# Kernel optimization log

Hardware: AMD Instinct MI355X
Metric: run time of the kernel (lower is better)

Reference implementation:

```python
import jax, jax.numpy as jnp
import numpy as np

DIM = 2048; H = 16; DK = 128; DV = 128; SEQ = 2048; KCONV = 4
KEY_DIM = H * DK; VAL_DIM = H * DV
EPS_L2 = 1e-6; EPS_RMS = 1e-6; SP_THRESH = 20.0


def setup_inputs() -> dict:
    key = jax.random.key(0)
    ks = jax.random.split(key, 20)
    f = jnp.float32
    def w(k, shape, scale):
        return jax.random.normal(k, shape, f) * scale
    s_in = DIM ** -0.5
    return {
        "x": jax.random.normal(ks[0], (1, SEQ, DIM), f),
        "ve": jax.random.normal(ks[1], (1, SEQ, H, DV), f),
        "sa_lambdas": jnp.array([0.7, 0.3], f),
        "Wq": w(ks[2], (DIM, KEY_DIM), s_in),
        "Wk": w(ks[3], (DIM, KEY_DIM), s_in),
        "Wv": w(ks[4], (DIM, VAL_DIM), s_in),
        "conv_q": w(ks[5], (KEY_DIM, KCONV), 0.5),
        "conv_k": w(ks[6], (KEY_DIM, KCONV), 0.5),
        "conv_v": w(ks[7], (VAL_DIM, KCONV), 0.5),
        "Wf1": w(ks[8], (DIM, DV), s_in),
        "Wf2": w(ks[9], (DV, KEY_DIM), DV ** -0.5),
        "Wb": w(ks[10], (DIM, H), s_in),
        "A_log": jnp.log(jax.random.uniform(ks[11], (H,), f, 1.0, 16.0)),
        "dt_bias": jnp.zeros((KEY_DIM,), f),
        "Wg1": w(ks[12], (DIM, DV), s_in),
        "Wg2": w(ks[13], (DV, VAL_DIM), DV ** -0.5),
        "bg2": jnp.zeros((VAL_DIM,), f),
        "norm_w": jnp.ones((DV,), f),
        "Wo": w(ks[14], (VAL_DIM, DIM), VAL_DIM ** -0.5),
    }


def _short_conv_silu(u, w):
    # u: [b, s, c], w: [c, K]; causal depthwise conv + silu
    s = u.shape[1]
    up = jnp.pad(u, ((0, 0), (w.shape[1] - 1, 0), (0, 0)))
    y = sum(up[:, i:i + s, :] * w[:, i] for i in range(w.shape[1]))
    return jax.nn.silu(y)


def _l2norm(t):
    return t * jax.lax.rsqrt(jnp.sum(t * t, axis=-1, keepdims=True) + EPS_L2)


def _forward(x, ve, sa_lambdas, Wq, Wk, Wv, conv_q, conv_k, conv_v,
             Wf1, Wf2, Wb, A_log, dt_bias, Wg1, Wg2, bg2, norm_w, Wo):
    b, s, _ = x.shape  # b == 1
    q = _short_conv_silu(x @ Wq, conv_q).reshape(b, s, H, DK)
    k = _short_conv_silu(x @ Wk, conv_k).reshape(b, s, H, DK)
    v = _short_conv_silu(x @ Wv, conv_v).reshape(b, s, H, DV)
    v = sa_lambdas[0] * v + sa_lambdas[1] * ve
    # KDA gate: per-(head, key-dim) log decay
    g = ((x @ Wf1) @ Wf2).reshape(b, s, H, DK) + dt_bias.reshape(H, DK)
    sp = jnp.where(g > SP_THRESH, g, jnp.log1p(jnp.exp(jnp.minimum(g, SP_THRESH))))
    glog = -jnp.exp(A_log)[None, None, :, None] * sp  # [b,s,h,dk]
    beta = jax.nn.sigmoid(x @ Wb)  # [b,s,h]
    # l2-normalize q,k; scale q by dk^-0.5 (chunk_kda default scale)
    qn = _l2norm(q) * (DK ** -0.5)
    kn = _l2norm(k)
    # gated delta-rule recurrence over time (b==1, squeeze batch)
    def step(S, inp):
        qt, kt, vt, gt, bt = inp  # [h,dk],[h,dk],[h,dv],[h,dk],[h]
        S = S * jnp.exp(gt)[..., None]  # per-key-channel decay
        pred = jnp.einsum('hk,hkv->hv', kt, S)
        vt_new = bt[:, None] * (vt - pred)
        S = S + kt[:, :, None] * vt_new[:, None, :]
        ot = jnp.einsum('hk,hkv->hv', qt, S)
        return S, ot
    S0 = jnp.zeros((H, DK, DV), x.dtype)
    _, o = jax.lax.scan(step, S0, (qn[0], kn[0], v[0], glog[0], beta[0]))
    o = o[None]  # [1,s,h,dv]
    # sigmoid-gated RMSNorm over head_v_dim
    gate = ((x @ Wg1) @ Wg2 + bg2).reshape(b, s, H, DV)
    var = jnp.mean(o * o, axis=-1, keepdims=True)
    o = o * jax.lax.rsqrt(var + EPS_RMS) * norm_w
    o = o * jax.nn.sigmoid(gate)
    return o.reshape(b, s, VAL_DIM) @ Wo  # [1,s,dim]


def reference(x, ve, sa_lambdas, Wq, Wk, Wv, conv_q, conv_k, conv_v,
              Wf1, Wf2, Wb, A_log, dt_bias, Wg1, Wg2, bg2, norm_w, Wo):
    return _forward(x, ve, sa_lambdas, Wq, Wk, Wv, conv_q, conv_k, conv_v,
                    Wf1, Wf2, Wb, A_log, dt_bias, Wg1, Wg2, bg2, norm_w, Wo)
```

## Files before the change

kernel.cpp:

```cpp
#include <hip/hip_runtime.h>
#include <hip/hip_bf16.h>
#include <stdint.h>
#include <stddef.h>

#define SEQL 2048
#define DIMSZ 2048
#define HN 16
#define DKD 128
#define DVD 128
#define QSCALE 0.08838834764831843f

typedef __attribute__((ext_vector_type(4))) float f32x4;
typedef __attribute__((ext_vector_type(2))) float f32x2;
typedef __attribute__((ext_vector_type(8))) short bf16x8;

__device__ __forceinline__ float sigmoid_f(float x) { return 1.f / (1.f + __expf(-x)); }
__device__ __forceinline__ float bf2f(short s) {
  union { float f; unsigned int u; } t; t.u = ((unsigned int)(unsigned short)s) << 16; return t.f;
}

#define BM 128
#define BN 128
#define BKK 64

// ... 113 lines not shown
          const int kc = ks * 4 + l4;
          a[m2][ks] = *(const bf16x8*)(lds + cb + la * 64 + (kc ^ (la & 7)) * 8);
        }
    }
#pragma unroll
    for (int ks = 0; ks < 2; ++ks) {
      const int lb = NQ * 64 + wn * 16 + l15;
      const int kc = ks * 4 + l4;
      b[ks] = *(const bf16x8*)(lds + cb + 16384 + lb * 64 + (kc ^ (lb & 7)) * 8);
    }
    __builtin_amdgcn_s_setprio(1);
#pragma unroll
    for (int m2 = 0; m2 < 4; ++m2)
#pragma unroll
      for (int ks = 0; ks < 2; ++ks)
        acc[MQ * 4 + m2][NQ] = __builtin_amdgcn_mfma_f32_16x16x32_bf16(
            a[m2][ks], b[ks], acc[MQ * 4 + m2][NQ], 0, 0, 0);
    __builtin_amdgcn_s_setprio(0);
  };

  stage_a(0, 0); stage_a(1, 0); stage_b(0, 0); stage_b(1, 0); stage_b(2, 0);

  for (int t = 0; t < NT; ++t) {
    const size_t cb = (size_t)(t & 1) * 28672;
    stage_a(0, t + 1);
    asm volatile("s_waitcnt vmcnt(4)" ::: "memory");
    __builtin_amdgcn_s_barrier();
    __builtin_amdgcn_sched_barrier(0);
    phase(cb, 0, 0, true);
    __builtin_amdgcn_s_barrier();
    stage_a(1, t + 1);
    asm volatile("s_waitcnt vmcnt(5)" ::: "memory");
    __builtin_amdgcn_s_barrier();
    __builtin_amdgcn_sched_barrier(0);
    phase(cb, 0, 1, false);
    __builtin_amdgcn_s_barrier();
    stage_b(0, t + 1);
    asm volatile("s_waitcnt vmcnt(5)" ::: "memory");
    __builtin_amdgcn_s_barrier();
    __builtin_amdgcn_sched_barrier(0);
    phase(cb, 0, 2, false);
    __builtin_amdgcn_s_barrier();
    stage_b(1, t + 1);
    __builtin_amdgcn_s_barrier();
    __builtin_amdgcn_sched_barrier(0);
    phase(cb, 1, 0, true);
    __builtin_amdgcn_s_barrier();
    stage_b(2, t + 1);
    __builtin_amdgcn_s_barrier();
    __builtin_amdgcn_sched_barrier(0);
    phase(cb, 1, 1, false);
    __builtin_amdgcn_s_barrier();
    __builtin_amdgcn_s_barrier();
    __builtin_amdgcn_sched_barrier(0);
    phase(cb, 1, 2, false);
    __builtin_amdgcn_s_barrier();
  }
  asm volatile("s_waitcnt vmcnt(0)" ::: "memory");

#pragma unroll
  for (int mi = 0; mi < 8; ++mi)
#pragma unroll
    for (int nq = 0; nq < 3; ++nq) {
      const int row = m0 + wm * 128 + mi * 16 + l4 * 4;
      const int col = n0 + nq * 64 + wn * 16 + l15;
#pragma unroll
      for (int r = 0; r < 4; ++r)
        Cb[(size_t)(row + r) * N + col] = __float2bfloat16(acc[mi][nq][r]);
    }
}

__global__ __launch_bounds__(256) void gemm_btsplit(
    const __hip_bfloat16* __restrict__ Ah, const __hip_bfloat16* __restrict__ Al,
    const __hip_bfloat16* __restrict__ Bh, const __hip_bfloat16* __restrict__ Bl,
    float* __restrict__ C, int M, int N, int lda, int ldb, int klen)
{
  __shared__ __hip_bfloat16 Ash[BM * BKK];
  __shared__ __hip_bfloat16 Asl[BM * BKK];
  __shared__ __hip_bfloat16 Bsh[BN * BKK];
  __shared__ __hip_bfloat16 Bsl[BN * BKK];
  const int tid = threadIdx.x;
  const int lane = tid & 63;
  const int w = tid >> 6;
  const int wm = w >> 1, wn = w & 1;
  const int m0 = blockIdx.y * BM, n0 = blockIdx.x * BN;
  const int l15 = lane & 15, l4 = lane >> 4;
  const int kbase = blockIdx.z * klen;

  f32x4 acc[4][4] = {};

  for (int k0 = kbase; k0 < kbase + klen; k0 += BKK) {
#pragma unroll
    for (int i = 0; i < 4; ++i) {
      const int c = (w * 4 + i) * 64 + lane;
      const int row = c >> 3;
      const int colb = (c & 7) * 8;
      const size_t go = (size_t)(m0 + row) * lda + k0 + colb;
      const size_t gn = (size_t)(n0 + row) * ldb + k0 + colb;
      __builtin_amdgcn_global_load_lds(
          (const __attribute__((address_space(1))) void*)(Ah + go),
          (__attribute__((address_space(3))) void*)(Ash + (size_t)c * 8), 16, 0, 0);
      __builtin_amdgcn_global_load_lds(
          (const __attribute__((address_space(1))) void*)(Al + go),
          (__attribute__((address_space(3))) void*)(Asl + (size_t)c * 8), 16, 0, 0);
      __builtin_amdgcn_global_load_lds(
          (const __attribute__((address_space(1))) void*)(Bh + gn),
          (__attribute__((address_space(3))) void*)(Bsh + (size_t)c * 8), 16, 0, 0);
      __builtin_amdgcn_global_load_lds(
          (const __attribute__((address_space(1))) void*)(Bl + gn),
          (__attribute__((address_space(3))) void*)(Bsl + (size_t)c * 8), 16, 0, 0);
    }
    __syncthreads();
#pragma unroll
    for (int kk = 0; kk < BKK; kk += 32) {
      bf16x8 afh[4], afl[4], bfh[4], bfl[4];
#pragma unroll
      for (int mi = 0; mi < 4; ++mi) {
        const int ao = (wm * 64 + mi * 16 + l15) * BKK + kk + l4 * 8;
        afh[mi] = *(const bf16x8*)(Ash + ao);
        afl[mi] = *(const bf16x8*)(Asl + ao);
      }
#pragma unroll
      for (int ni = 0; ni < 4; ++ni) {
        const int bo = (wn * 64 + ni * 16 + l15) * BKK + kk + l4 * 8;
        bfh[ni] = *(const bf16x8*)(Bsh + bo);
        bfl[ni] = *(const bf16x8*)(Bsl + bo);
      }
#pragma unroll
      for (int mi = 0; mi < 4; ++mi)
#pragma unroll
        for (int ni = 0; ni < 4; ++ni) {
          acc[mi][ni] = __builtin_amdgcn_mfma_f32_16x16x32_bf16(afh[mi], bfh[ni], acc[mi][ni], 0, 0, 0);
          acc[mi][ni] = __builtin_amdgcn_mfma_f32_16x16x32_bf16(afh[mi], bfl[ni], acc[mi][ni], 0, 0, 0);
          acc[mi][ni] = __builtin_amdgcn_mfma_f32_16x16x32_bf16(afl[mi], bfh[ni], acc[mi][ni], 0, 0, 0);
        }
    }
    __syncthreads();
  }

  float* Cz = C + (size_t)blockIdx.z * M * N;
#pragma unroll
  for (int mi = 0; mi < 4; ++mi) {
#pragma unroll
    for (int ni = 0; ni < 4; ++ni) {
      const int row = m0 + wm * 64 + mi * 16 + l4 * 4;
      const int col = n0 + wn * 64 + ni * 16 + l15;
#pragma unroll
      for (int r = 0; r < 4; ++r)
        Cz[(size_t)(row + r) * N + col] = acc[mi][ni][r];
    }
  }
}

__global__ __launch_bounds__(256) void transpose4_kernel(
    const float* __restrict__ Wq, const float* __restrict__ Wk,
    const float* __restrict__ Wv, const float* __restrict__ Wo,
    __hip_bfloat16* __restrict__ WqkvT, __hip_bfloat16* __restrict__ WoT)
{
  __shared__ float tile[32][33];
  const int z = blockIdx.z;
  const float* in = (z == 0) ? Wq : (z == 1) ? Wk : (z == 2) ? Wv : Wo;
  __hip_bfloat16* outT = (z < 3) ? (WqkvT + (size_t)z * 2048 * 2048) : WoT;
  const int c0 = blockIdx.x * 32, r0 = blockIdx.y * 32;
  const int tc = threadIdx.x & 31, tr = threadIdx.x >> 5;
#pragma unroll
  for (int i = 0; i < 4; ++i)
    tile[tr + i * 8][tc] = in[(size_t)(r0 + tr + i * 8) * 2048 + c0 + tc];
  __syncthreads();
#pragma unroll
  for (int i = 0; i < 4; ++i)
    outT[(size_t)(c0 + tr + i * 8) * 2048 + r0 + tc] = __float2bfloat16(tile[tc][tr + i * 8]);
}

__global__ __launch_bounds__(256) void transpose_fg1_kernel(
    const float* __restrict__ Wf1, const float* __restrict__ Wg1,
    __hip_bfloat16* __restrict__ hT, __hip_bfloat16* __restrict__ lT)
{
  __shared__ float tile[32][33];
  const int z = blockIdx.z;
  const float* in = z ? Wg1 : Wf1;
  const size_t base = (size_t)z * 128 * 2048;
  const int c0 = blockIdx.x * 32, r0 = blockIdx.y * 32;
  const int tc = threadIdx.x & 31, tr = threadIdx.x >> 5;
#pragma unroll
  for (int i = 0; i < 4; ++i)
    tile[tr + i * 8][tc] = in[(size_t)(r0 + tr + i * 8) * 128 + c0 + tc];
  __syncthreads();
#pragma unroll
  for (int i = 0; i < 4; ++i) {
    float val = tile[tc][tr + i * 8];
    __hip_bfloat16 h = __float2bfloat16(val);
    size_t oi = base + (size_t)(c0 + tr + i * 8) * 2048 + r0 + tc;
    hT[oi] = h;
    lT[oi] = z ? __float2bfloat16(0.f) : __float2bfloat16(val - __bfloat162float(h));
  }
}

__global__ __launch_bounds__(256) void transpose_f2g2_kernel(
    const float* __restrict__ Wf2, const float* __restrict__ Wg2,
    __hip_bfloat16* __restrict__ f2h, __hip_bfloat16* __restrict__ f2l,
    __hip_bfloat16* __restrict__ g2h)
{
  __shared__ float tile[32][33];
  const int z = blockIdx.z;
  const float* in = z ? Wg2 : Wf2;
  const int c0 = blockIdx.x * 32, r0 = blockIdx.y * 32;
  const int tc = threadIdx.x & 31, tr = threadIdx.x >> 5;
#pragma unroll
  for (int i = 0; i < 4; ++i)
    tile[tr + i * 8][tc] = in[(size_t)(r0 + tr + i * 8) * 2048 + c0 + tc];
  __syncthreads();
#pragma unroll
  for (int i = 0; i < 4; ++i) {
    float val = tile[tc][tr + i * 8];
    __hip_bfloat16 h = __float2bfloat16(val);
    size_t oi = (size_t)(c0 + tr + i * 8) * 128 + r0 + tc;
    if (z == 0) { f2h[oi] = h; f2l[oi] = __float2bfloat16(val - __bfloat162float(h)); }
    else g2h[oi] = h;
  }
}

__global__ __launch_bounds__(256) void cast_split_kernel(
    const float* __restrict__ in, __hip_bfloat16* __restrict__ hi,
    __hip_bfloat16* __restrict__ lo, int n4)
{
  int idx = blockIdx.x * 256 + threadIdx.x;
  if (idx >= n4) return;
  f32x4 v = *(const f32x4*)(in + (size_t)idx * 4);
  union { __hip_bfloat16 b[4]; unsigned long long u; } ph, pl;
#pragma unroll
  for (int j = 0; j < 4; ++j) {
    float f = v[j];
    __hip_bfloat16 hh = __float2bfloat16(f);
    ph.b[j] = hh;
    pl.b[j] = __float2bfloat16(f - __bfloat162float(hh));
  }
  *(unsigned long long*)((char*)hi + (size_t)idx * 8) = ph.u;
  if (lo) *(unsigned long long*)((char*)lo + (size_t)idx * 8) = pl.u;
}

__global__ __launch_bounds__(256) void reduce8_kernel(
    const float* __restrict__ part, __hip_bfloat16* __restrict__ hi,
    __hip_bfloat16* __restrict__ lo, int n4, size_t chunk)
{
  int idx = blockIdx.x * 256 + threadIdx.x;
  if (idx >= n4) return;
  f32x4 a = *(const f32x4*)(part + (size_t)idx * 4);
#pragma unroll
  for (int z = 1; z < 8; ++z) {
    f32x4 b = *(const f32x4*)(part + z * chunk + (size_t)idx * 4);
    a.x += b.x; a.y += b.y; a.z += b.z; a.w += b.w;
  }
  union { __hip_bfloat16 b[4]; unsigned long long u; } ph, pl;
#pragma unroll
  for (int j = 0; j < 4; ++j) {
    float f = a[j];
    __hip_bfloat16 hh = __float2bfloat16(f);
    ph.b[j] = hh;
    pl.b[j] = __float2bfloat16(f - __bfloat162float(hh));
  }
  *(unsigned long long*)((char*)hi + (size_t)idx * 8) = ph.u;
  if (lo) *(unsigned long long*)((char*)lo + (size_t)idx * 8) = pl.u;
}

__global__ __launch_bounds__(256) void beta_kernel(
    const float* __restrict__ x, const float* __restrict__ Wb, float* __restrict__ betaT)
{
  int idx = blockIdx.x * 256 + threadIdx.x;
  int s = idx >> 4, h = idx & 15;
  const float* xr = x + (size_t)s * DIMSZ;
  float acc = 0.f;
  for (int d = 0; d < DIMSZ; d += 4) {
    f32x4 xv = *(const f32x4*)(xr + d);
    acc = fmaf(xv.x, Wb[(size_t)(d + 0) * HN + h], acc);
    acc = fmaf(xv.y, Wb[(size_t)(d + 1) * HN + h], acc);
    acc = fmaf(xv.z, Wb[(size_t)(d + 2) * HN + h], acc);
    acc = fmaf(xv.w, Wb[(size_t)(d + 3) * HN + h], acc);
  }
  betaT[(size_t)h * SEQL + s] = 1.f / (1.f + expf(-acc));
}

#define SL20(r, d) ((r) * 160 + ((d) >> 4) * 20 + ((d) & 15))

__global__ __launch_bounds__(256) void kda_pref(
    const __hip_bfloat16* __restrict__ qkv, const float* __restrict__ ve,
    const float* __restrict__ lam,
    const float* __restrict__ cwq, const float* __restrict__ cwk, const float* __restrict__ cwv,
    const float* __restrict__ gbuf,
    const float* __restrict__ dtb, const float* __restrict__ A_log,
    const float* __restrict__ betaT,
    __hip_bfloat16* __restrict__ Xgh, __hip_bfloat16* __restrict__ KTh,
    float* __restrict__ uvS, float* __restrict__ olocS, float* __restrict__ Pg)
{
  __shared__ float GL2[32 * 160];
  __shared__ float kL2[32 * 160];
  __shared__ float qL2[32 * 132];
  __shared__ float vL2[32 * 128];
  __shared__ float ALB[32][33];
  __shared__ float Bdiag[32], betaL[32];
  __shared__ float csumW[4 * 128];

  const int bid = blockIdx.x;
  const int h = bid >> 6, cc = bid & 63;
  const int tid = threadIdx.x;
  const int w = tid >> 6, lane = tid & 63;
  const size_t hc = (size_t)h * 64 + cc;
  const float Aexp = __expf(A_log[h]);

  {
    const int c = lane * 2;
    const int r0g = cc * 32 + w * 8;
    const int cg = h * 128 + c;

    f32x4 wq0 = *(const f32x4*)(cwq + (size_t)cg * 4), wq1 = *(const f32x4*)(cwq + (size_t)(cg + 1) * 4);
    f32x4 wk0 = *(const f32x4*)(cwk + (size_t)cg * 4), wk1 = *(const f32x4*)(cwk + (size_t)(cg + 1) * 4);
    f32x4 wv0 = *(const f32x4*)(cwv + (size_t)cg * 4), wv1 = *(const f32x4*)(cwv + (size_t)(cg + 1) * 4);
    f32x2 dt2 = *(const f32x2*)(dtb + cg);
    const float l0 = lam[0], l1 = lam[1];

    f32x2 xqr[11], xkr[11], xvr[11];
#pragma unroll
    for (int i = 0; i < 11; ++i) {
      const int sr = r0g - 3 + i;
      if (sr >= 0) {
        const size_t ro = (size_t)sr * 6144 + cg;
        unsigned int uq = *(const unsigned int*)(qkv + ro);
        unsigned int uk = *(const unsigned int*)(qkv + 2048 + ro);
        unsigned int uv2 = *(const unsigned int*)(qkv + 4096 + ro);
        xqr[i].x = bf2f((short)uq);   xqr[i].y = bf2f((short)(uq >> 16));
        xkr[i].x = bf2f((short)uk);   xkr[i].y = bf2f((short)(uk >> 16));
        xvr[i].x = bf2f((short)uv2);  xvr[i].y = bf2f((short)(uv2 >> 16));
      } else {
        xqr[i].x = xqr[i].y = xkr[i].x = xkr[i].y = xvr[i].x = xvr[i].y = 0.f;
      }
    }

    float gl0[8], gl1[8];
#pragma unroll
    for (int i = 0; i < 8; ++i) {
      const int rr = r0g + i;
      const int lr = w * 8 + i;
      float aq0 = 0, aq1 = 0, ak0 = 0, ak1 = 0, av0 = 0, av1 = 0;
#pragma unroll
      for (int j = 0; j < 4; ++j) {
        aq0 = fmaf(xqr[i + j].x, wq0[j], aq0); aq1 = fmaf(xqr[i + j].y, wq1[j], aq1);
        ak0 = fmaf(xkr[i + j].x, wk0[j], ak0); ak1 = fmaf(xkr[i + j].y, wk1[j], ak1);
        av0 = fmaf(xvr[i + j].x, wv0[j], av0); av1 = fmaf(xvr[i + j].y, wv1[j], av1);
      }
      float yq0 = aq0 * sigmoid_f(aq0), yq1 = aq1 * sigmoid_f(aq1);
      float yk0 = ak0 * sigmoid_f(ak0), yk1 = ak1 * sigmoid_f(ak1);
      float yv0 = av0 * sigmoid_f(av0), yv1 = av1 * sigmoid_f(av1);

      f32x2 vev = *(const f32x2*)(ve + ((size_t)rr * HN + h) * 128 + c);
      float v0 = l0 * yv0 + l1 * vev.x;
      float v1 = l0 * yv1 + l1 * vev.y;

      float ssq = yq0 * yq0 + yq1 * yq1;
      float ssk = yk0 * yk0 + yk1 * yk1;
#pragma unroll
      for (int off = 32; off > 0; off >>= 1) {
        ssq += __shfl_xor(ssq, off);
        ssk += __shfl_xor(ssk, off);
      }
      float rq = rsqrtf(ssq + 1e-6f) * QSCALE;
      float rk = rsqrtf(ssk + 1e-6f);

      f32x2 kk; kk.x = yk0 * rk; kk.y = yk1 * rk;
      f32x2 qq; qq.x = yq0 * rq; qq.y = yq1 * rq;
      f32x2 vv; vv.x = v0; vv.y = v1;
      *(f32x2*)&kL2[SL20(lr, c)] = kk;
      *(f32x2*)&qL2[lr * 132 + c] = qq;
      *(f32x2*)&vL2[lr * 128 + c] = vv;

      f32x2 gv = *(const f32x2*)(gbuf + (size_t)rr * 2048 + cg);
      float g0 = gv.x + dt2.x, g1 = gv.y + dt2.y;
      float sp0 = (g0 > 20.f) ? g0 : log1pf(__expf(fminf(g0, 20.f)));
      float sp1 = (g1 > 20.f) ? g1 : log1pf(__expf(fminf(g1, 20.f)));
      gl0[i] = -Aexp * sp0;
      gl1[i] = -Aexp * sp1;
    }
    {
      float r0 = 0.f, r1 = 0.f;
#pragma unroll
      for (int i = 0; i < 8; ++i) { r0 += gl0[i]; gl0[i] = r0; r1 += gl1[i]; gl1[i] = r1; }
      csumW[w * 128 + c] = r0;
      csumW[w * 128 + c + 1] = r1;
    }
    if (tid < 32) betaL[tid] = betaT[(size_t)h * SEQL + cc * 32 + tid];
    __syncthreads();
    {
      float p0 = 0.f, p1 = 0.f;
      for (int wp = 0; wp < w; ++wp) { p0 += csumW[wp * 128 + c]; p1 += csumW[wp * 128 + c + 1]; }
#pragma unroll
      for (int i = 0; i < 8; ++i) {
        f32x2 gg; gg.x = gl0[i] + p0; gg.y = gl1[i] + p1;
        *(f32x2*)&GL2[SL20(w * 8 + i, c)] = gg;
      }
    }
  }
  __syncthreads();

  {
    const int tg = lane >> 3, s8 = lane & 7;
    const int tt = w * 8 + tg;
    const int ds = s8 * 20;

    float Gt[16], kt[16], qt[16];
#pragma unroll
    for (int j = 0; j < 16; j += 4) {
      *(f32x4*)&Gt[j] = *(const f32x4*)&GL2[tt * 160 + ds + j];
      *(f32x4*)&kt[j] = *(const f32x4*)&kL2[tt * 160 + ds + j];
      *(f32x4*)&qt[j] = *(const f32x4*)&qL2[tt * 132 + s8 * 16 + j];
    }
    {
      float sA = 0.f, sB = 0.f;
#pragma unroll
      for (int j = 0; j < 16; ++j) { sA = fmaf(kt[j], kt[j], sA); sB = fmaf(qt[j], kt[j], sB); }
      sA += __shfl_xor(sA, 1); sA += __shfl_xor(sA, 2); sA += __shfl_xor(sA, 4);
      sB += __shfl_xor(sB, 1); sB += __shfl_xor(sB, 2); sB += __shfl_xor(sB, 4);
      if (s8 == 0) { ALB[tt][tt] = sA; Bdiag[tt] = sB; }
    }
    const int ibound = w * 8 + 7;
    for (int i = 0; i < ibound; ++i) {
      if (i < tt) {
        float sA = 0.f, sB = 0.f;
#pragma unroll
        for (int jj = 0; jj < 4; ++jj) {
          f32x4 Gi = *(const f32x4*)&GL2[i * 160 + ds + jj * 4];
          f32x4 ki = *(const f32x4*)&kL2[i * 160 + ds + jj * 4];
#pragma unroll
          for (int u = 0; u < 4; ++u) {
            float e = __expf(Gt[jj * 4 + u] - Gi[u]);
            float kid = ki[u] * e;
            sA = fmaf(kt[jj * 4 + u], kid, sA);
            sB = fmaf(qt[jj * 4 + u], kid, sB);
          }
        }
        sA += __shfl_xor(sA, 1); sA += __shfl_xor(sA, 2); sA += __shfl_xor(sA, 4);
        sB += __shfl_xor(sB, 1); sB += __shfl_xor(sB, 2); sB += __shfl_xor(sB, 4);
        if (s8 == 0) { ALB[tt][i] = sA; ALB[i][tt] = sB; }
      }
    }
  }
  __syncthreads();

  const int col = tid & 127, half = tid >> 7;
  const size_t rowbase = (size_t)(cc * 32) * 2048 + h * 128 + col;
  const int rbase = half * 16;
  {
    const float g31 = GL2[SL20(31, col)];
    size_t kb = hc * 4096 + (size_t)col * 32;
#pragma unroll
    for (int i = 0; i < 16; ++i) {
      int r = rbase + i;
      float kv = kL2[SL20(r, col)] * __expf(g31 - GL2[SL20(r, col)]);
      KTh[kb + r] = __float2bfloat16(kv);
    }
  }

  if (half == 0) {
    float expg[32];
#pragma unroll
    for (int r = 0; r < 32; ++r) expg[r] = __expf(GL2[SL20(r, col)]);

    float uvr[32], wr[32];
#pragma unroll
    for (int r = 0; r < 32; ++r) {
      float suv = 0.f, sw = 0.f;
#pragma unroll
      for (int j = 0; j < 32; ++j) {
        if (j < r) { float a = ALB[r][j]; suv = fmaf(a, uvr[j], suv); sw = fmaf(a, wr[j], sw); }
      }
      float br = betaL[r];
      float khr = kL2[SL20(r, col)] * expg[r];
      uvr[r] = br * (vL2[r * 128 + col] - suv);
      wr[r] = br * (khr - sw);
      uvS[rowbase + (size_t)r * 2048] = uvr[r];
      Xgh[hc * 8192 + (size_t)(32 + r) * 128 + col] = __float2bfloat16(wr[r]);
    }

#pragma unroll
    for (int r = 0; r < 32; ++r) {
      float qtv = qL2[r * 132 + col] * expg[r];
      float ol = 0.f;
#pragma unroll
      for (int j = 0; j < 32; ++j) {
        if (j < r) { float b = ALB[j][r]; qtv = fmaf(-b, wr[j], qtv); ol = fmaf(b, uvr[j], ol); }
      }
      { float b = Bdiag[r]; qtv = fmaf(-b, wr[r], qtv); ol = fmaf(b, uvr[r], ol); }
      Xgh[hc * 8192 + (size_t)r * 128 + col] = __float2bfloat16(qtv);
      olocS[rowbase + (size_t)r * 2048] = ol;
    }
    Pg[hc * 128 + col] = expg[31];
  }
}

#define STP 136
#define UTP 40

struct ChunkOps {
  bf16x8 ah[4];
  bf16x8 kah[2];
  f32x4 pvv[2];
  float pB[4];
};

__global__ __launch_bounds__(256) void kda_seq(
    const __hip_bfloat16* __restrict__ Xgh, const __hip_bfloat16* __restrict__ KTh,
    const float* __restrict__ uvS, const float* __restrict__ olocS,
    const float* __restrict__ Pg, float* __restrict__ obuf)
{
  __shared__ __hip_bfloat16 STh[16 * STP], STl[16 * STP];
  __shared__ __hip_bfloat16 UTh[16 * UTP];
  const int tid = threadIdx.x;
  const int w = tid >> 6, lane = tid & 63, l15 = lane & 15, l4 = lane >> 4;
  const int h = blockIdx.x >> 3, vq = blockIdx.x & 7;
  const int v0 = vq * 16;
  const int r0 = (w & 1) * 16 + l4 * 4;
  const int isO = (w < 2);

  for (int i = tid; i < 16 * STP; i += 256) {
    STh[i] = __float2bfloat16(0.f);
    STl[i] = __float2bfloat16(0.f);
  }
  __syncthreads();

  f32x4 S[2] = {};

  auto loadops = [&](ChunkOps& o, int c) {
    const size_t hc = (size_t)h * 64 + c;
    const __hip_bfloat16* xh = Xgh + hc * 8192 + (size_t)(w * 16 + l15) * 128 + l4 * 8;
#pragma unroll
    for (int kk = 0; kk < 4; ++kk) o.ah[kk] = *(const bf16x8*)(xh + kk * 32);
    const float* pb = (isO ? olocS : uvS) + (size_t)(c * 32 + r0) * 2048 + h * 128 + v0 + l15;
#pragma unroll
    for (int r = 0; r < 4; ++r) o.pB[r] = pb[(size_t)r * 2048];
#pragma unroll
    for (int mi = 0; mi < 2; ++mi) {
      const int kd = (w * 2 + mi) * 16;
      o.kah[mi] = *(const bf16x8*)(KTh + hc * 4096 + (size_t)(kd + l15) * 32 + l4 * 8);
      o.pvv[mi] = *(const f32x4*)(Pg + hc * 128 + kd + l4 * 4);
    }
  };

  auto body = [&](ChunkOps& o, int c) {
    f32x4 Y = {};
#pragma unroll
    for (int kk = 0; kk < 4; ++kk) {
      const int so = l15 * STP + kk * 32 + l4 * 8;
      bf16x8 bh = *(const bf16x8*)(STh + so);
      bf16x8 bl = *(const bf16x8*)(STl + so);
      Y = __builtin_amdgcn_mfma_f32_16x16x32_bf16(o.ah[kk], bh, Y, 0, 0, 0);
      Y = __builtin_amdgcn_mfma_f32_16x16x32_bf16(o.ah[kk], bl, Y, 0, 0, 0);
    }

    if (isO) {
      size_t ob = (size_t)(c * 32 + r0) * 2048 + h * 128 + v0 + l15;
#pragma unroll
      for (int r = 0; r < 4; ++r)
        obuf[ob + (size_t)r * 2048] = Y[r] + o.pB[r];
    } else {
      union { __hip_bfloat16 b[4]; unsigned long long u; } uh;
#pragma unroll
      for (int r = 0; r < 4; ++r)
        uh.b[r] = __float2bfloat16(o.pB[r] - Y[r]);
      *(unsigned long long*)(UTh + l15 * UTP + r0) = uh.u;
    }
    __syncthreads();

#pragma unroll
    for (int mi = 0; mi < 2; ++mi) S[mi] *= o.pvv[mi];
    {
      bf16x8 ubh = *(const bf16x8*)(UTh + l15 * UTP + l4 * 8);
#pragma unroll
      for (int mi = 0; mi < 2; ++mi)
        S[mi] = __builtin_amdgcn_mfma_f32_16x16x32_bf16(o.kah[mi], ubh, S[mi], 0, 0, 0);
    }

#pragma unroll
    for (int mi = 0; mi < 2; ++mi) {
      const int kd0 = (w * 2 + mi) * 16 + l4 * 4;
      union { __hip_bfloat16 b[4]; unsigned long long u; } sh, sl;
#pragma unroll
      for (int r = 0; r < 4; ++r) {
        __hip_bfloat16 hh = __float2bfloat16(S[mi][r]);
        sh.b[r] = hh;
        sl.b[r] = __float2bfloat16(S[mi][r] - __bfloat162float(hh));
      }
      *(unsigned long long*)(STh + l15 * STP + kd0) = sh.u;
      *(unsigned long long*)(STl + l15 * STP + kd0) = sl.u;
    }
    __syncthreads();
  };

  ChunkOps A_, B_;
  loadops(A_, 0);
  for (int c = 0; c < 64; c += 2) {
    loadops(B_, c + 1);
    body(A_, c);
    if (c + 2 < 64) loadops(A_, c + 2);
    body(B_, c + 1);
  }
}

__global__ __launch_bounds__(256) void rmsgate_kernel(
    const float* __restrict__ o, const float* __restrict__ gate,
    const float* __restrict__ bg2, const float* __restrict__ norm_w,
    __hip_bfloat16* __restrict__ og)
{
  int row = blockIdx.x * 4 + (threadIdx.x >> 6);
  int lane = threadIdx.x & 63;
  int s = row >> 4, h = row & 15;
  int j = lane * 2;
  const float* p = o + (size_t)row * 128 + j;
  f32x2 v = *(const f32x2*)p;
  float ss = v.x * v.x + v.y * v.y;
#pragma unroll
  for (int off = 32; off > 0; off >>= 1) ss += __shfl_xor(ss, off);
  float rs = rsqrtf(ss * (1.f / 128.f) + 1e-6f);
  int c = h * 128 + j;
  float g0 = gate[(size_t)s * 2048 + c] + bg2[c];
  float g1 = gate[(size_t)s * 2048 + c + 1] + bg2[c + 1];
  float o0 = v.x * rs * norm_w[j] * (1.f / (1.f + expf(-g0)));
  float o1 = v.y * rs * norm_w[j + 1] * (1.f / (1.f + expf(-g1)));
  union { __hip_bfloat16 b[2]; unsigned int u; } pk2;
  pk2.b[0] = __float2bfloat16(o0);
  pk2.b[1] = __float2bfloat16(o1);
  *(unsigned int*)((char*)og + ((size_t)s * 2048 + c) * 2) = pk2.u;
}

extern "C" void kernel_launch(void* const* d_in, const int* in_sizes, int n_in,
                              void* d_out, int out_size, void* d_ws, size_t ws_size,
                              hipStream_t stream)
{
  const float* x      = (const float*)d_in[0];
  const float* ve     = (const float*)d_in[1];
  const float* lam    = (const float*)d_in[2];
  const float* Wq     = (const float*)d_in[3];
  const float* Wk     = (const float*)d_in[4];
  const float* Wv     = (const float*)d_in[5];
  const float* cwq    = (const float*)d_in[6];
  const float* cwk    = (const float*)d_in[7];
  const float* cwv    = (const float*)d_in[8];
  const float* Wf1    = (const float*)d_in[9];
  const float* Wf2    = (const float*)d_in[10];
  const float* Wb     = (const float*)d_in[11];
  const float* A_log  = (const float*)d_in[12];
  const float* dtb    = (const float*)d_in[13];
  const float* Wg1    = (const float*)d_in[14];
  const float* Wg2    = (const float*)d_in[15];
  const float* bg2    = (const float*)d_in[16];
  const float* norm_w = (const float*)d_in[17];
  const float* Wo     = (const float*)d_in[18];
  float* out = (float*)d_out;

  const size_t S2 = (size_t)2048 * 2048;

  char* p = (char*)d_ws;
  auto alloc = [&](size_t bytes) { char* r = p; p += (bytes + 255) & ~(size_t)255; return r; };

  __hip_bfloat16* xb     = (__hip_bfloat16*)alloc(S2 * 2);
  __hip_bfloat16* WoT    = (__hip_bfloat16*)alloc(S2 * 2);
  __hip_bfloat16* Wf2hT  = (__hip_bfloat16*)alloc(2048 * 128 * 2);
  __hip_bfloat16* Wf2lT  = (__hip_bfloat16*)alloc(2048 * 128 * 2);
  __hip_bfloat16* Wg2T   = (__hip_bfloat16*)alloc(2048 * 128 * 2);
  __hip_bfloat16* Wfg1hT = (__hip_bfloat16*)alloc((size_t)256 * 2048 * 2);
  __hip_bfloat16* Wfg1lT = (__hip_bfloat16*)alloc((size_t)256 * 2048 * 2);
  __hip_bfloat16* f1g1h  = (__hip_bfloat16*)alloc((size_t)2048 * 256 * 2);
  __hip_bfloat16* f1g1l  = (__hip_bfloat16*)alloc((size_t)2048 * 256 * 2);
  float* betaT = (float*)alloc((size_t)2048 * 16 * 4);
  __hip_bfloat16* qkvb = (__hip_bfloat16*)alloc(3 * S2 * 2);
  float* gbuf  = (float*)alloc(S2 * 4);
  float* gatebuf = (float*)alloc(S2 * 4);
  float* uvS   = (float*)alloc(S2 * 4);
  float* olocS = (float*)alloc(S2 * 4);
  __hip_bfloat16* Xgh = (__hip_bfloat16*)alloc(S2 * 4);
  __hip_bfloat16* KTh = (__hip_bfloat16*)alloc(S2 * 2);
  float* Pg    = (float*)alloc((size_t)1024 * 128 * 4);

  __hip_bfloat16* WqkvT = (__hip_bfloat16*)uvS;
  __hip_bfloat16* xlo = (__hip_bfloat16*)((char*)olocS + S2 * 2);
  float* fpart = (float*)Xgh;
  float* obuf  = gbuf;
  __hip_bfloat16* og = (__hip_bfloat16*)qkvb;

  cast_split_kernel<<<4096, 256, 0, stream>>>(x, xb, xlo, (int)(S2 / 4));

  transpose4_kernel<<<dim3(64, 64, 4), 256, 0, stream>>>(Wq, Wk, Wv, Wo, WqkvT, WoT);
  transpose_fg1_kernel<<<dim3(4, 64, 2), 256, 0, stream>>>(Wf1, Wg1, Wfg1hT, Wfg1lT);
  transpose_f2g2_kernel<<<dim3(64, 4, 2), 256, 0, stream>>>(Wf2, Wg2, Wf2hT, Wf2lT, Wg2T);

  gemm_bt192<<<dim3(32, 8), 512, 0, stream>>>(xb, WqkvT, qkvb, 6144, 2048, 2048, 32);

  gemm_btsplit<<<dim3(2, 16, 8), 256, 0, stream>>>(xb, xlo, Wfg1hT, Wfg1lT, fpart,
                                                   2048, 256, 2048, 2048, 256);
  reduce8_kernel<<<512, 256, 0, stream>>>(fpart, f1g1h, f1g1l, 131072, (size_t)2048 * 256);

  gemm_btsplit<<<dim3(16, 16), 256, 0, stream>>>(f1g1h, f1g1l, Wf2hT, Wf2lT, gbuf,
                                                 2048, 2048, 256, 128, 128);
  gemm_bt<<<dim3(16, 16), 256, 0, stream>>>(f1g1h + 128, Wg2T, gatebuf,
                                            2048, 2048, 256, 128, 128, 0);

  beta_kernel<<<128, 256, 0, stream>>>(x, Wb, betaT);

  kda_pref<<<1024, 256, 0, stream>>>(qkvb, ve, lam, cwq, cwk, cwv, gbuf, dtb, A_log, betaT,
                                     Xgh, KTh, uvS, olocS, Pg);

  kda_seq<<<128, 256, 0, stream>>>(Xgh, KTh, uvS, olocS, Pg, obuf);

  rmsgate_kernel<<<8192, 256, 0, stream>>>(obuf, gatebuf, bg2, norm_w, og);

  gemm_bt<<<dim3(16, 16), 256, 0, stream>>>(og, WoT, out, 2048, 2048, 2048, 2048, 2048, 0);
}
```

Baseline: 375.5 us.

## Merge prep kernels and overlap gate GEMM with sequential KDA recurrence

The four weight and input preparation kernels are merged into one launch with branching on block index. The beta projection moves into the reduce8 kernel as extra blocks. The gate GEMM (g1 @ Wg2) now runs as extra blocks inside the sequential KDA recurrence kernel, so it uses CUs left idle by that kernel's 128 blocks. The aim is fewer launches and better use of the GPU during the latency-bound scan. The cost is a shared 64KB LDS allocation for every block, which could lower occupancy for the recurrence blocks.

```diff
diff --git a/kernel.cpp b/kernel.cpp
--- a/kernel.cpp
+++ b/kernel.cpp
@@ -289,132 +289,123 @@
   }
 }
 
-__global__ __launch_bounds__(256) void transpose4_kernel(
+__global__ __launch_bounds__(256) void prep_all_kernel(
+    const float* __restrict__ x, __hip_bfloat16* __restrict__ xb, __hip_bfloat16* __restrict__ xlo,
     const float* __restrict__ Wq, const float* __restrict__ Wk,
     const float* __restrict__ Wv, const float* __restrict__ Wo,
-    __hip_bfloat16* __restrict__ WqkvT, __hip_bfloat16* __restrict__ WoT)
-{
-  __shared__ float tile[32][33];
-  const int z = blockIdx.z;
-  const float* in = (z == 0) ? Wq : (z == 1) ? Wk : (z == 2) ? Wv : Wo;
-  __hip_bfloat16* outT = (z < 3) ? (WqkvT + (size_t)z * 2048 * 2048) : WoT;
-  const int c0 = blockIdx.x * 32, r0 = blockIdx.y * 32;
-  const int tc = threadIdx.x & 31, tr = threadIdx.x >> 5;
-#pragma unroll
-  for (int i = 0; i < 4; ++i)
-    tile[tr + i * 8][tc] = in[(size_t)(r0 + tr + i * 8) * 2048 + c0 + tc];
-  __syncthreads();
-#pragma unroll
-  for (int i = 0; i < 4; ++i)
-    outT[(size_t)(c0 + tr + i * 8) * 2048 + r0 + tc] = __float2bfloat16(tile[tc][tr + i * 8]);
-}
-
-__global__ __launch_bounds__(256) void transpose_fg1_kernel(
+    __hip_bfloat16* __restrict__ WqkvT, __hip_bfloat16* __restrict__ WoT,
     const float* __restrict__ Wf1, const float* __restrict__ Wg1,
-    __hip_bfloat16* __restrict__ hT, __hip_bfloat16* __restrict__ lT)
-{
-  __shared__ float tile[32][33];
-  const int z = blockIdx.z;
-  const float* in = z ? Wg1 : Wf1;
-  const size_t base = (size_t)z * 128 * 2048;
-  const int c0 = blockIdx.x * 32, r0 = blockIdx.y * 32;
-  const int tc = threadIdx.x & 31, tr = threadIdx.x >> 5;
-#pragma unroll
-  for (int i = 0; i < 4; ++i)
-    tile[tr + i * 8][tc] = in[(size_t)(r0 + tr + i * 8) * 128 + c0 + tc];
-  __syncthreads();
-#pragma unroll
-  for (int i = 0; i < 4; ++i) {
-    float val = tile[tc][tr + i * 8];
-    __hip_bfloat16 h = __float2bfloat16(val);
-    size_t oi = base + (size_t)(c0 + tr + i * 8) * 2048 + r0 + tc;
-    hT[oi] = h;
-    lT[oi] = z ? __float2bfloat16(0.f) : __float2bfloat16(val - __bfloat162float(h));
-  }
-}
-
-__global__ __launch_bounds__(256) void transpose_f2g2_kernel(
+    __hip_bfloat16* __restrict__ fg1h, __hip_bfloat16* __restrict__ fg1l,
     const float* __restrict__ Wf2, const float* __restrict__ Wg2,
     __hip_bfloat16* __restrict__ f2h, __hip_bfloat16* __restrict__ f2l,
     __hip_bfloat16* __restrict__ g2h)
 {
   __shared__ float tile[32][33];
-  const int z = blockIdx.z;
-  const float* in = z ? Wg2 : Wf2;
-  const int c0 = blockIdx.x * 32, r0 = blockIdx.y * 32;
-  const int tc = threadIdx.x & 31, tr = threadIdx.x >> 5;
-#pragma unroll
-  for (int i = 0; i < 4; ++i)
-    tile[tr + i * 8][tc] = in[(size_t)(r0 + tr + i * 8) * 2048 + c0 + tc];
-  __syncthreads();
-#pragma unroll
-  for (int i = 0; i < 4; ++i) {
-    float val = tile[tc][tr + i * 8];
-    __hip_bfloat16 h = __float2bfloat16(val);
-    size_t oi = (size_t)(c0 + tr + i * 8) * 128 + r0 + tc;
-    if (z == 0) { f2h[oi] = h; f2l[oi] = __float2bfloat16(val - __bfloat162float(h)); }
-    else g2h[oi] = h;
-  }
-}
-
-__global__ __launch_bounds__(256) void cast_split_kernel(
-    const float* __restrict__ in, __hip_bfloat16* __restrict__ hi,
-    __hip_bfloat16* __restrict__ lo, int n4)
-{
-  int idx = blockIdx.x * 256 + threadIdx.x;
-  if (idx >= n4) return;
-  f32x4 v = *(const f32x4*)(in + (size_t)idx * 4);
-  union { __hip_bfloat16 b[4]; unsigned long long u; } ph, pl;
-#pragma unroll
-  for (int j = 0; j < 4; ++j) {
-    float f = v[j];
-    __hip_bfloat16 hh = __float2bfloat16(f);
-    ph.b[j] = hh;
-    pl.b[j] = __float2bfloat16(f - __bfloat162float(hh));
-  }
-  *(unsigned long long*)((char*)hi + (size_t)idx * 8) = ph.u;
-  if (lo) *(unsigned long long*)((char*)lo + (size_t)idx * 8) = pl.u;
-}
-
-__global__ __launch_bounds__(256) void reduce8_kernel(
+  const int bid = blockIdx.x;
+  const int tid = threadIdx.x;
+  const int tc = tid & 31, tr = tid >> 5;
+
+  if (bid < 16384) {
+    const int z = bid >> 12, rem = bid & 4095;
+    const int c0 = (rem & 63) * 32, r0 = (rem >> 6) * 32;
+    const float* in = (z == 0) ? Wq : (z == 1) ? Wk : (z == 2) ? Wv : Wo;
+    __hip_bfloat16* outT = (z < 3) ? (WqkvT + (size_t)z * 2048 * 2048) : WoT;
+#pragma unroll
+    for (int i = 0; i < 4; ++i)
+      tile[tr + i * 8][tc] = in[(size_t)(r0 + tr + i * 8) * 2048 + c0 + tc];
+    __syncthreads();
+#pragma unroll
+    for (int i = 0; i < 4; ++i)
+      outT[(size_t)(c0 + tr + i * 8) * 2048 + r0 + tc] = __float2bfloat16(tile[tc][tr + i * 8]);
+  } else if (bid < 16896) {
+    const int rem = bid - 16384;
+    const int z = rem >> 8, within = rem & 255;
+    const int c0 = (within & 3) * 32, r0 = (within >> 2) * 32;
+    const float* in = z ? Wg1 : Wf1;
+    const size_t base = (size_t)z * 128 * 2048;
+#pragma unroll
+    for (int i = 0; i < 4; ++i)
+      tile[tr + i * 8][tc] = in[(size_t)(r0 + tr + i * 8) * 128 + c0 + tc];
+    __syncthreads();
+#pragma unroll
+    for (int i = 0; i < 4; ++i) {
+      float val = tile[tc][tr + i * 8];
+      __hip_bfloat16 h = __float2bfloat16(val);
+      size_t oi = base + (size_t)(c0 + tr + i * 8) * 2048 + r0 + tc;
+      fg1h[oi] = h;
+      fg1l[oi] = z ? __float2bfloat16(0.f) : __float2bfloat16(val - __bfloat162float(h));
+    }
+  } else if (bid < 17408) {
+    const int rem = bid - 16896;
+    const int z = rem >> 8, within = rem & 255;
+    const int c0 = (within & 63) * 32, r0 = (within >> 6) * 32;
+    const float* in = z ? Wg2 : Wf2;
+#pragma unroll
+    for (int i = 0; i < 4; ++i)
+      tile[tr + i * 8][tc] = in[(size_t)(r0 + tr + i * 8) * 2048 + c0 + tc];
+    __syncthreads();
+#pragma unroll
+    for (int i = 0; i < 4; ++i) {
+      float val = tile[tc][tr + i * 8];
+      __hip_bfloat16 h = __float2bfloat16(val);
+      size_t oi = (size_t)(c0 + tr + i * 8) * 128 + r0 + tc;
+      if (z == 0) { f2h[oi] = h; f2l[oi] = __float2bfloat16(val - __bfloat162float(h)); }
+      else g2h[oi] = h;
+    }
+  } else {
+    const int idx = (bid - 17408) * 256 + tid;
+    f32x4 v = *(const f32x4*)(x + (size_t)idx * 4);
+    union { __hip_bfloat16 b[4]; unsigned long long u; } ph, pl;
+#pragma unroll
+    for (int j = 0; j < 4; ++j) {
+      float f = v[j];
+      __hip_bfloat16 hh = __float2bfloat16(f);
+      ph.b[j] = hh;
+      pl.b[j] = __float2bfloat16(f - __bfloat162float(hh));
+    }
+    *(unsigned long long*)((char*)xb + (size_t)idx * 8) = ph.u;
+    *(unsigned long long*)((char*)xlo + (size_t)idx * 8) = pl.u;
+  }
+}
+
+__global__ __launch_bounds__(256) void reduce8_beta_kernel(
     const float* __restrict__ part, __hip_bfloat16* __restrict__ hi,
-    __hip_bfloat16* __restrict__ lo, int n4, size_t chunk)
-{
-  int idx = blockIdx.x * 256 + threadIdx.x;
-  if (idx >= n4) return;
-  f32x4 a = *(const f32x4*)(part + (size_t)idx * 4);
-#pragma unroll
-  for (int z = 1; z < 8; ++z) {
-    f32x4 b = *(const f32x4*)(part + z * chunk + (size_t)idx * 4);
-    a.x += b.x; a.y += b.y; a.z += b.z; a.w += b.w;
-  }
-  union { __hip_bfloat16 b[4]; unsigned long long u; } ph, pl;
-#pragma unroll
-  for (int j = 0; j < 4; ++j) {
-    float f = a[j];
-    __hip_bfloat16 hh = __float2bfloat16(f);
-    ph.b[j] = hh;
-    pl.b[j] = __float2bfloat16(f - __bfloat162float(hh));
-  }
-  *(unsigned long long*)((char*)hi + (size_t)idx * 8) = ph.u;
-  if (lo) *(unsigned long long*)((char*)lo + (size_t)idx * 8) = pl.u;
-}
-
-__global__ __launch_bounds__(256) void beta_kernel(
+    __hip_bfloat16* __restrict__ lo, size_t chunk,
     const float* __restrict__ x, const float* __restrict__ Wb, float* __restrict__ betaT)
 {
-  int idx = blockIdx.x * 256 + threadIdx.x;
-  int s = idx >> 4, h = idx & 15;
-  const float* xr = x + (size_t)s * DIMSZ;
-  float acc = 0.f;
-  for (int d = 0; d < DIMSZ; d += 4) {
-    f32x4 xv = *(const f32x4*)(xr + d);
-    acc = fmaf(xv.x, Wb[(size_t)(d + 0) * HN + h], acc);
-    acc = fmaf(xv.y, Wb[(size_t)(d + 1) * HN + h], acc);
-    acc = fmaf(xv.z, Wb[(size_t)(d + 2) * HN + h], acc);
-    acc = fmaf(xv.w, Wb[(size_t)(d + 3) * HN + h], acc);
-  }
-  betaT[(size_t)h * SEQL + s] = 1.f / (1.f + expf(-acc));
+  const int tid = threadIdx.x;
+  if (blockIdx.x < 512) {
+    int idx = blockIdx.x * 256 + tid;
+    f32x4 a = *(const f32x4*)(part + (size_t)idx * 4);
+#pragma unroll
+    for (int z = 1; z < 8; ++z) {
+      f32x4 b = *(const f32x4*)(part + z * chunk + (size_t)idx * 4);
+      a.x += b.x; a.y += b.y; a.z += b.z; a.w += b.w;
+    }
+    union { __hip_bfloat16 b[4]; unsigned long long u; } ph, pl;
+#pragma unroll
+    for (int j = 0; j < 4; ++j) {
+      float f = a[j];
+      __hip_bfloat16 hh = __float2bfloat16(f);
+      ph.b[j] = hh;
+      pl.b[j] = __float2bfloat16(f - __bfloat162float(hh));
+    }
+    *(unsigned long long*)((char*)hi + (size_t)idx * 8) = ph.u;
+    *(unsigned long long*)((char*)lo + (size_t)idx * 8) = pl.u;
+  } else {
+    int idx = (blockIdx.x - 512) * 256 + tid;
+    int s = idx >> 4, h = idx & 15;
+    const float* xr = x + (size_t)s * DIMSZ;
+    float acc = 0.f;
+    for (int d = 0; d < DIMSZ; d += 4) {
+      f32x4 xv = *(const f32x4*)(xr + d);
+      acc = fmaf(xv.x, Wb[(size_t)(d + 0) * HN + h], acc);
+      acc = fmaf(xv.y, Wb[(size_t)(d + 1) * HN + h], acc);
+      acc = fmaf(xv.z, Wb[(size_t)(d + 2) * HN + h], acc);
+      acc = fmaf(xv.w, Wb[(size_t)(d + 3) * HN + h], acc);
+    }
+    betaT[(size_t)h * SEQL + s] = 1.f / (1.f + expf(-acc));
+  }
 }
 
 #define SL20(r, d) ((r) * 160 + ((d) >> 4) * 20 + ((d) & 15))
@@ -642,101 +633,159 @@
   float pB[4];
 };
 
-__global__ __launch_bounds__(256) void kda_seq(
+__global__ __launch_bounds__(256) void kda_seq_gate(
     const __hip_bfloat16* __restrict__ Xgh, const __hip_bfloat16* __restrict__ KTh,
     const float* __restrict__ uvS, const float* __restrict__ olocS,
-    const float* __restrict__ Pg, float* __restrict__ obuf)
+    const float* __restrict__ Pg, float* __restrict__ obuf,
+    const __hip_bfloat16* __restrict__ g1b, const __hip_bfloat16* __restrict__ Wg2T,
+    float* __restrict__ gatebuf)
 {
-  __shared__ __hip_bfloat16 STh[16 * STP], STl[16 * STP];
-  __shared__ __hip_bfloat16 UTh[16 * UTP];
+  __shared__ char smem[65536];
   const int tid = threadIdx.x;
   const int w = tid >> 6, lane = tid & 63, l15 = lane & 15, l4 = lane >> 4;
-  const int h = blockIdx.x >> 3, vq = blockIdx.x & 7;
-  const int v0 = vq * 16;
-  const int r0 = (w & 1) * 16 + l4 * 4;
-  const int isO = (w < 2);
-
-  for (int i = tid; i < 16 * STP; i += 256) {
-    STh[i] = __float2bfloat16(0.f);
-    STl[i] = __float2bfloat16(0.f);
-  }
-  __syncthreads();
-
-  f32x4 S[2] = {};
-
-  auto loadops = [&](ChunkOps& o, int c) {
-    const size_t hc = (size_t)h * 64 + c;
-    const __hip_bfloat16* xh = Xgh + hc * 8192 + (size_t)(w * 16 + l15) * 128 + l4 * 8;
-#pragma unroll
-    for (int kk = 0; kk < 4; ++kk) o.ah[kk] = *(const bf16x8*)(xh + kk * 32);
-    const float* pb = (isO ? olocS : uvS) + (size_t)(c * 32 + r0) * 2048 + h * 128 + v0 + l15;
-#pragma unroll
-    for (int r = 0; r < 4; ++r) o.pB[r] = pb[(size_t)r * 2048];
-#pragma unroll
-    for (int mi = 0; mi < 2; ++mi) {
-      const int kd = (w * 2 + mi) * 16;
-      o.kah[mi] = *(const bf16x8*)(KTh + hc * 4096 + (size_t)(kd + l15) * 32 + l4 * 8);
-      o.pvv[mi] = *(const f32x4*)(Pg + hc * 128 + kd + l4 * 4);
-    }
-  };
-
-  auto body = [&](ChunkOps& o, int c) {
-    f32x4 Y = {};
-#pragma unroll
-    for (int kk = 0; kk < 4; ++kk) {
-      const int so = l15 * STP + kk * 32 + l4 * 8;
-      bf16x8 bh = *(const bf16x8*)(STh + so);
-      bf16x8 bl = *(const bf16x8*)(STl + so);
-      Y = __builtin_amdgcn_mfma_f32_16x16x32_bf16(o.ah[kk], bh, Y, 0, 0, 0);
-      Y = __builtin_amdgcn_mfma_f32_16x16x32_bf16(o.ah[kk], bl, Y, 0, 0, 0);
-    }
-
-    if (isO) {
-      size_t ob = (size_t)(c * 32 + r0) * 2048 + h * 128 + v0 + l15;
-#pragma unroll
-      for (int r = 0; r < 4; ++r)
-        obuf[ob + (size_t)r * 2048] = Y[r] + o.pB[r];
-    } else {
-      union { __hip_bfloat16 b[4]; unsigned long long u; } uh;
-#pragma unroll
-      for (int r = 0; r < 4; ++r)
-        uh.b[r] = __float2bfloat16(o.pB[r] - Y[r]);
-      *(unsigned long long*)(UTh + l15 * UTP + r0) = uh.u;
+
+  if (blockIdx.x < 128) {
+    __hip_bfloat16* STh = (__hip_bfloat16*)smem;
+    __hip_bfloat16* STl = STh + 16 * STP;
+    __hip_bfloat16* UTh = STl + 16 * STP;
+    const int h = blockIdx.x >> 3, vq = blockIdx.x & 7;
+    const int v0 = vq * 16;
+    const int r0 = (w & 1) * 16 + l4 * 4;
+    const int isO = (w < 2);
+
+    for (int i = tid; i < 16 * STP; i += 256) {
+      STh[i] = __float2bfloat16(0.f);
+      STl[i] = __float2bfloat16(0.f);
     }
     __syncthreads();
 
-#pragma unroll
-    for (int mi = 0; mi < 2; ++mi) S[mi] *= o.pvv[mi];
-    {
-      bf16x8 ubh = *(const bf16x8*)(UTh + l15 * UTP + l4 * 8);
-#pragma unroll
-      for (int mi = 0; mi < 2; ++mi)
-        S[mi] = __builtin_amdgcn_mfma_f32_16x16x32_bf16(o.kah[mi], ubh, S[mi], 0, 0, 0);
-    }
-
-#pragma unroll
-    for (int mi = 0; mi < 2; ++mi) {
-      const int kd0 = (w * 2 + mi) * 16 + l4 * 4;
-      union { __hip_bfloat16 b[4]; unsigned long long u; } sh, sl;
-#pragma unroll
-      for (int r = 0; r < 4; ++r) {
-        __hip_bfloat16 hh = __float2bfloat16(S[mi][r]);
-        sh.b[r] = hh;
-        sl.b[r] = __float2bfloat16(S[mi][r] - __bfloat162float(hh));
-      }
-      *(unsigned long long*)(STh + l15 * STP + kd0) = sh.u;
-      *(unsigned long long*)(STl + l15 * STP + kd0) = sl.u;
-    }
-    __syncthreads();
-  };
-
-  ChunkOps A_, B_;
-  loadops(A_, 0);
-  for (int c = 0; c < 64; c += 2) {
-    loadops(B_, c + 1);
-    body(A_, c);
-    if (c + 2 < 64) loadops(A_, c + 2);
-    body(B_, c + 1);
+    f32x4 S[2] = {};
+
+    auto loadops = [&](ChunkOps& o, int c) {
+      const size_t hc = (size_t)h * 64 + c;
+      const __hip_bfloat16* xh = Xgh + hc * 8192 + (size_t)(w * 16 + l15) * 128 + l4 * 8;
+#pragma unroll
+      for (int kk = 0; kk < 4; ++kk) o.ah[kk] = *(const bf16x8*)(xh + kk * 32);
+      const float* pb = (isO ? olocS : uvS) + (size_t)(c * 32 + r0) * 2048 + h * 128 + v0 + l15;
+#pragma unroll
+      for (int r = 0; r < 4; ++r) o.pB[r] = pb[(size_t)r * 2048];
+#pragma unroll
+      for (int mi = 0; mi < 2; ++mi) {
+        const int kd = (w * 2 + mi) * 16;
+        o.kah[mi] = *(const bf16x8*)(KTh + hc * 4096 + (size_t)(kd + l15) * 32 + l4 * 8);
+        o.pvv[mi] = *(const f32x4*)(Pg + hc * 128 + kd + l4 * 4);
+      }
+    };
+
+    auto body = [&](ChunkOps& o, int c) {
+      f32x4 Y = {};
+#pragma unroll
+      for (int kk = 0; kk < 4; ++kk) {
+        const int so = l15 * STP + kk * 32 + l4 * 8;
+        bf16x8 bh = *(const bf16x8*)(STh + so);
+        bf16x8 bl = *(const bf16x8*)(STl + so);
+        Y = __builtin_amdgcn_mfma_f32_16x16x32_bf16(o.ah[kk], bh, Y, 0, 0, 0);
+        Y = __builtin_amdgcn_mfma_f32_16x16x32_bf16(o.ah[kk], bl, Y, 0, 0, 0);
+      }
+
+      if (isO) {
+        size_t ob = (size_t)(c * 32 + r0) * 2048 + h * 128 + v0 + l15;
+#pragma unroll
+        for (int r = 0; r < 4; ++r)
+          obuf[ob + (size_t)r * 2048] = Y[r] + o.pB[r];
+      } else {
+        union { __hip_bfloat16 b[4]; unsigned long long u; } uh;
+#pragma unroll
+        for (int r = 0; r < 4; ++r)
+          uh.b[r] = __float2bfloat16(o.pB[r] - Y[r]);
+        *(unsigned long long*)(UTh + l15 * UTP + r0) = uh.u;
+      }
+      __syncthreads();
+
+#pragma unroll
+      for (int mi = 0; mi < 2; ++mi) S[mi] *= o.pvv[mi];
+      {
+        bf16x8 ubh = *(const bf16x8*)(UTh + l15 * UTP + l4 * 8);
+#pragma unroll
+        for (int mi = 0; mi < 2; ++mi)
+          S[mi] = __builtin_amdgcn_mfma_f32_16x16x32_bf16(o.kah[mi], ubh, S[mi], 0, 0, 0);
+      }
+
+#pragma unroll
+      for (int mi = 0; mi < 2; ++mi) {
+        const int kd0 = (w * 2 + mi) * 16 + l4 * 4;
+        union { __hip_bfloat16 b[4]; unsigned long long u; } sh, sl;
+#pragma unroll
+        for (int r = 0; r < 4; ++r) {
+          __hip_bfloat16 hh = __float2bfloat16(S[mi][r]);
+          sh.b[r] = hh;
+          sl.b[r] = __float2bfloat16(S[mi][r] - __bfloat162float(hh));
+        }
+        *(unsigned long long*)(STh + l15 * STP + kd0) = sh.u;
+        *(unsigned long long*)(STl + l15 * STP + kd0) = sl.u;
+      }
+      __syncthreads();
+    };
+
+    ChunkOps A_, B_;
+    loadops(A_, 0);
+    for (int c = 0; c < 64; c += 2) {
+      loadops(B_, c + 1);
+      body(A_, c);
+      if (c + 2 < 64) loadops(A_, c + 2);
+      body(B_, c + 1);
+    }
+  } else {
+    __hip_bfloat16* As = (__hip_bfloat16*)smem;
+    __hip_bfloat16* Bs = As + BM * BKK;
+    const int b2 = blockIdx.x - 128;
+    const int m0 = (b2 >> 4) * BM, n0 = (b2 & 15) * BN;
+    const int wm = w >> 1, wn = w & 1;
+
+    f32x4 acc[4][4] = {};
+
+    for (int k0 = 0; k0 < 128; k0 += BKK) {
+#pragma unroll
+      for (int i = 0; i < 4; ++i) {
+        const int c = (w * 4 + i) * 64 + lane;
+        const int row = c >> 3;
+        const int colb = (c & 7) * 8;
+        __builtin_amdgcn_global_load_lds(
+            (const __attribute__((address_space(1))) void*)(g1b + (size_t)(m0 + row) * 256 + k0 + colb),
+            (__attribute__((address_space(3))) void*)(As + (size_t)c * 8), 16, 0, 0);
+        __builtin_amdgcn_global_load_lds(
+            (const __attribute__((address_space(1))) void*)(Wg2T + (size_t)(n0 + row) * 128 + k0 + colb),
+            (__attribute__((address_space(3))) void*)(Bs + (size_t)c * 8), 16, 0, 0);
+      }
+      __syncthreads();
+#pragma unroll
+      for (int kk = 0; kk < BKK; kk += 32) {
+        bf16x8 af[4], bfv[4];
+#pragma unroll
+        for (int mi = 0; mi < 4; ++mi)
+          af[mi] = *(const bf16x8*)(As + (wm * 64 + mi * 16 + l15) * BKK + kk + l4 * 8);
+#pragma unroll
+        for (int ni = 0; ni < 4; ++ni)
+          bfv[ni] = *(const bf16x8*)(Bs + (wn * 64 + ni * 16 + l15) * BKK + kk + l4 * 8);
+#pragma unroll
+        for (int mi = 0; mi < 4; ++mi)
+#pragma unroll
+          for (int ni = 0; ni < 4; ++ni)
+            acc[mi][ni] = __builtin_amdgcn_mfma_f32_16x16x32_bf16(af[mi], bfv[ni], acc[mi][ni], 0, 0, 0);
+      }
+      __syncthreads();
+    }
+
+#pragma unroll
+    for (int mi = 0; mi < 4; ++mi)
+#pragma unroll
+      for (int ni = 0; ni < 4; ++ni) {
+        const int row = m0 + wm * 64 + mi * 16 + l4 * 4;
+        const int col = n0 + wn * 64 + ni * 16 + l15;
+#pragma unroll
+        for (int r = 0; r < 4; ++r)
+          gatebuf[(size_t)(row + r) * 2048 + col] = acc[mi][ni][r];
+      }
   }
 }
 
@@ -821,29 +870,25 @@
   float* obuf  = gbuf;
   __hip_bfloat16* og = (__hip_bfloat16*)qkvb;
 
-  cast_split_kernel<<<4096, 256, 0, stream>>>(x, xb, xlo, (int)(S2 / 4));
-
-  transpose4_kernel<<<dim3(64, 64, 4), 256, 0, stream>>>(Wq, Wk, Wv, Wo, WqkvT, WoT);
-  transpose_fg1_kernel<<<dim3(4, 64, 2), 256, 0, stream>>>(Wf1, Wg1, Wfg1hT, Wfg1lT);
-  transpose_f2g2_kernel<<<dim3(64, 4, 2), 256, 0, stream>>>(Wf2, Wg2, Wf2hT, Wf2lT, Wg2T);
+  prep_all_kernel<<<21504, 256, 0, stream>>>(x, xb, xlo, Wq, Wk, Wv, Wo, WqkvT, WoT,
+                                             Wf1, Wg1, Wfg1hT, Wfg1lT,
+                                             Wf2, Wg2, Wf2hT, Wf2lT, Wg2T);
 
   gemm_bt192<<<dim3(32, 8), 512, 0, stream>>>(xb, WqkvT, qkvb, 6144, 2048, 2048, 32);
 
   gemm_btsplit<<<dim3(2, 16, 8), 256, 0, stream>>>(xb, xlo, Wfg1hT, Wfg1lT, fpart,
                                                    2048, 256, 2048, 2048, 256);
-  reduce8_kernel<<<512, 256, 0, stream>>>(fpart, f1g1h, f1g1l, 131072, (size_t)2048 * 256);
+  reduce8_beta_kernel<<<640, 256, 0, stream>>>(fpart, f1g1h, f1g1l, (size_t)2048 * 256,
+                                               x, Wb, betaT);
 
   gemm_btsplit<<<dim3(16, 16), 256, 0, stream>>>(f1g1h, f1g1l, Wf2hT, Wf2lT, gbuf,
                                                  2048, 2048, 256, 128, 128);
-  gemm_bt<<<dim3(16, 16), 256, 0, stream>>>(f1g1h + 128, Wg2T, gatebuf,
-                                            2048, 2048, 256, 128, 128, 0);
-
-  beta_kernel<<<128, 256, 0, stream>>>(x, Wb, betaT);
 
   kda_pref<<<1024, 256, 0, stream>>>(qkvb, ve, lam, cwq, cwk, cwv, gbuf, dtb, A_log, betaT,
                                      Xgh, KTh, uvS, olocS, Pg);
 
-  kda_seq<<<128, 256, 0, stream>>>(Xgh, KTh, uvS, olocS, Pg, obuf);
+  kda_seq_gate<<<384, 256, 0, stream>>>(Xgh, KTh, uvS, olocS, Pg, obuf,
+                                        f1g1h + 128, Wg2T, gatebuf);
 
   rmsgate_kernel<<<8192, 256, 0, stream>>>(obuf, gatebuf, bg2, norm_w, og);
 
```

Measured after the change: 360.8 us. 1.04x faster.
